# Performance work log

Measured on AMD Instinct MI355X. Metric: run time of the kernel, lower is better.

## Reference

```python
import jax, jax.numpy as jnp
import numpy as np

B, S, H, NH = 2, 2048, 2048, 16
HD = H // NH  # head_dim = 128


def setup_inputs() -> dict:
    key = jax.random.key(0)
    ks = jax.random.split(key, 6)
    scale = 1.0 / np.sqrt(H)
    hidden_state = jax.random.normal(ks[0], (B, S, H), dtype=jnp.float32)
    # upper-triangular (strictly above diagonal) = 1 -> masked positions
    causal_mask = jnp.triu(jnp.ones((S, S), dtype=jnp.float32), k=1)[None, None]
    Wq = jax.random.normal(ks[1], (H, H), dtype=jnp.float32) * scale
    Wk = jax.random.normal(ks[2], (H, H), dtype=jnp.float32) * scale
    Wv = jax.random.normal(ks[3], (H, H), dtype=jnp.float32) * scale
    Wo = jax.random.normal(ks[4], (H, H), dtype=jnp.float32) * scale
    zeros = jnp.zeros((H,), dtype=jnp.float32)
    return {"hidden_state": hidden_state, "causal_mask": causal_mask,
            "Wq": Wq, "bq": zeros, "Wk": Wk, "bk": zeros,
            "Wv": Wv, "bv": zeros, "Wo": Wo, "bo": zeros}


def reference(hidden_state, causal_mask, Wq, bq, Wk, bk, Wv, bv, Wo, bo):
    b, s, h = hidden_state.shape
    q = (hidden_state @ Wq.T + bq).reshape(b, s, NH, HD).transpose(0, 2, 1, 3)  # [B,NH,S,HD]
    k = (hidden_state @ Wk.T + bk).reshape(b, s, NH, HD).transpose(0, 2, 1, 3)
    v = (hidden_state @ Wv.T + bv).reshape(b, s, NH, HD).transpose(0, 2, 1, 3)
    scores = jnp.einsum('bhqd,bhkd->bhqk', q, k) / jnp.sqrt(jnp.float32(HD))
    scores = scores + causal_mask * (-1e9)
    probs = jax.nn.softmax(scores, axis=-1)
    out = jnp.einsum('bhqk,bhkd->bhqd', probs, v)
    out = out.transpose(0, 2, 1, 3).reshape(b, s, h)
    return out @ Wo.T + bo
```

## Files before the change

kernel.cpp:

```cpp
#include <hip/hip_runtime.h>
#include <hip/hip_bf16.h>
#include <stdint.h>

#define B_   2
#define S_   2048
#define H_   2048
#define NH_  16
#define HD_  128
#define MTOT (B_*S_)

typedef __attribute__((ext_vector_type(8))) short bf16x8;
typedef __attribute__((ext_vector_type(4))) float f32x4;

__device__ __forceinline__ void gload_lds16(const void* g, void* l) {
    __builtin_amdgcn_global_load_lds(
        (const __attribute__((address_space(1))) void*)g,
        (__attribute__((address_space(3))) void*)l, 16, 0, 0);
}

__device__ __forceinline__ unsigned short f2bfu(float x) {
    __hip_bfloat16 h = __float2bfloat16(x);
    return *reinterpret_cast<unsigned short*>(&h);
}
__device__ __forceinline__ int packbf(float a, float b) {
    return (int)f2bfu(a) | ((int)f2bfu(b) << 16);
}

__global__ void castk(const float* __restrict__ in, __hip_bfloat16* __restrict__ out, int n4) {
    int i = blockIdx.x * 256 + threadIdx.x;
    if (i < n4) {
        float4 v = *(const float4*)(in + (size_t)i * 4);
        out[(size_t)i*4 + 0] = __float2bfloat16(v.x);
        out[(size_t)i*4 + 1] = __float2bfloat16(v.y);
        out[(size_t)i*4 + 2] = __float2bfloat16(v.z);
        out[(size_t)i*4 + 3] = __float2bfloat16(v.w);
    }
}

__global__ void castw4(const float* __restrict__ w0, const float* __restrict__ w1,
                       const float* __restrict__ w2, const float* __restrict__ w3,
                       __hip_bfloat16* o0, __hip_bfloat16* o1,
                       __hip_bfloat16* o2, __hip_bfloat16* o3, int n4) {
    const float* in; __hip_bfloat16* out;
    switch (blockIdx.y) {
        case 0:  in = w0; out = o0; break;
        case 1:  in = w1; out = o1; break;
        case 2:  in = w2; out = o2; break;
        default: in = w3; out = o3; break;
    }
    int i = blockIdx.x * 256 + threadIdx.x;
    if (i < n4) {
        float4 v = *(const float4*)(in + (size_t)i * 4);
        out[(size_t)i*4 + 0] = __float2bfloat16(v.x);
        out[(size_t)i*4 + 1] = __float2bfloat16(v.y);
        out[(size_t)i*4 + 2] = __float2bfloat16(v.z);
        out[(size_t)i*4 + 3] = __float2bfloat16(v.w);
    }
}

template<int SMEMB, int BF16OUT>
__device__ __forceinline__ void gemm_body(const __hip_bfloat16* __restrict__ Ablk,
                                          const __hip_bfloat16* __restrict__ Wblk,
                                          const float* __restrict__ bias,
                                          void* __restrict__ Cout,
                                          int N, int K, int br, int bc, bool vt)
{
    __shared__ __align__(16) char smem[SMEMB];
    __hip_bfloat16* As = (__hip_bfloat16*)smem;
    __hip_bfloat16* Bs = (__hip_bfloat16*)(smem + 8192);

    const int tid  = threadIdx.x;
    const int wave = tid >> 6, lane = tid & 63;
    const int quad = lane >> 4, l16 = lane & 15;
    const int wr = wave >> 1, wc = wave & 1;

    f32x4 acc[4][4] = {};

    for (int k0 = 0; k0 < K; k0 += 32) {
#pragma unroll
        for (int t = 0; t < 2; ++t) {
            int c = t * 256 + wave * 64 + lane;
            int row = c >> 2, cc = c & 3;
            int base = (t * 256 + wave * 64) * 16;
            gload_lds16(Ablk + (size_t)row * K + k0 + cc * 8, (char*)As + base);
            gload_lds16(Wblk + (size_t)row * K + k0 + cc * 8, (char*)Bs + base);
        }
        __syncthreads();

        bf16x8 af[4], bf[4];
#pragma unroll
        for (int i = 0; i < 4; ++i)
            af[i] = *(const bf16x8*)&As[(wr * 64 + i * 16 + l16) * 32 + quad * 8];
#pragma unroll
        for (int j = 0; j < 4; ++j)
            bf[j] = *(const bf16x8*)&Bs[(wc * 64 + j * 16 + l16) * 32 + quad * 8];

#pragma unroll
        for (int i = 0; i < 4; ++i)
#pragma unroll
            for (int j = 0; j < 4; ++j)
                acc[i][j] = __builtin_amdgcn_mfma_f32_16x16x32_bf16(af[i], bf[j], acc[i][j], 0, 0, 0);
        __syncthreads();
    }

    if (BF16OUT && vt) {
        __hip_bfloat16* Ls = (__hip_bfloat16*)smem;
#pragma unroll
        for (int j = 0; j < 4; ++j) {
            int d = wc * 64 + j * 16 + l16;
            float bv = bias[bc * 128 + d];
#pragma unroll
            for (int i = 0; i < 4; ++i) {
                int t0 = wr * 64 + i * 16 + quad * 4;
#pragma unroll
                for (int r = 0; r < 4; ++r)
                    Ls[d * 136 + t0 + r] = __float2bfloat16(acc[i][j][r] + bv);
            }
        }
        __syncthreads();
        const int bq = br >> 4;
        const int s0 = (br & 15) * 128;
        __hip_bfloat16* VT = (__hip_bfloat16*)Cout;
        const size_t rowbase = (size_t)(bq * 16 + bc) * 128;
#pragma unroll
        for (int rep = 0; rep < 8; ++rep) {
            int L = rep * 256 + tid;
            int d = L >> 4, tch = L & 15;
            bf16x8 v = *(const bf16x8*)&Ls[d * 136 + tch * 8];
            *(bf16x8*)(VT + (rowbase + d) * (size_t)S_ + s0 + tch * 8) = v;
        }
        return;
    }

#pragma unroll
    for (int i = 0; i < 4; ++i) {
        int row = br * 128 + wr * 64 + i * 16 + quad * 4;
#pragma unroll
        for (int j = 0; j < 4; ++j) {
            int col = bc * 128 + wc * 64 + j * 16 + l16;
            float bv = bias[col];
#pragma unroll
            for (int r = 0; r < 4; ++r) {
                float v = acc[i][j][r] + bv;
                if (BF16OUT)
                    ((__hip_bfloat16*)Cout)[(size_t)(row + r) * N + col] = __float2bfloat16(v);
                else
                    ((float*)Cout)[(size_t)(row + r) * N + col] = v;
            }
        }
    }
}

__global__ __launch_bounds__(256)
void gemm_qkv(const __hip_bfloat16* __restrict__ X,
              const __hip_bfloat16* __restrict__ Wq, const __hip_bfloat16* __restrict__ Wk,
              const __hip_bfloat16* __restrict__ Wv,
              const float* __restrict__ bq, const float* __restrict__ bk,
              const float* __restrict__ bv,
              __hip_bfloat16* Qo, __hip_bfloat16* Ko, __hip_bfloat16* VTo)
{
    const int sel = blockIdx.x >> 4;
    const int bc  = blockIdx.x & 15;
    const int br  = blockIdx.y;
    const __hip_bfloat16* W = (sel == 0) ? Wq : (sel == 1) ? Wk : Wv;
    const float* bias       = (sel == 0) ? bq : (sel == 1) ? bk : bv;
    void* out               = (sel == 0) ? (void*)Qo : (sel == 1) ? (void*)Ko : (void*)VTo;
    gemm_body<34816, 1>(X + (size_t)(br * 128) * H_, W + (size_t)(bc * 128) * H_,
                        bias, out, H_, H_, br, bc, sel == 2);
}

__global__ __launch_bounds__(256)
void gemm_out(const __hip_bfloat16* __restrict__ A, const __hip_bfloat16* __restrict__ W,
              const float* __restrict__ bias, float* __restrict__ C)
{
    gemm_body<16384, 0>(A + (size_t)(blockIdx.y * 128) * H_, W + (size_t)(blockIdx.x * 128) * H_,
                        bias, C, H_, H_, blockIdx.y, blockIdx.x, false);
}

__global__ __launch_bounds__(256)
void attn_kernel(const __hip_bfloat16* __restrict__ Q,
                 const __hip_bfloat16* __restrict__ K,
                 const __hip_bfloat16* __restrict__ VT,
                 __hip_bfloat16* __restrict__ O)
{
    __shared__ __align__(16) char Ks[16384];
    __shared__ __align__(16) char Vt[16384];

    const int tid  = threadIdx.x;
    const int wave = tid >> 6, lane = tid & 63;
    const int quad = lane >> 4, l16 = lane & 15;

    const int lid = blockIdx.x;
    const int xcd = lid & 7;
    const int q   = lid >> 3;
    const int bh  = ((q >> 5) << 3) | xcd;
    const int qb  = 31 - (q & 31);
    const int b   = bh >> 4, h = bh & 15;

    const size_t headoff = (size_t)b * S_ * H_ + (size_t)h * HD_;
    const __hip_bfloat16* Qp  = Q + headoff;
    const __hip_bfloat16* Kp  = K + headoff;
    const __hip_bfloat16* Vtp = VT + (size_t)(b * 16 + h) * 128 * S_;

    const float scale = 0.08838834764831843f;
    const int A0 = (((quad & 1) * 2) * 16 + l16) * 4;
    const int A1 = A0 + 64;
    const bool hiq = (quad >= 2);

    const int qrow_local = wave * 16;
    const int qrow = qb * 64 + qrow_local;

    bf16x8 qf[4];
#pragma unroll
    for (int kd = 0; kd < 4; ++kd)
        qf[kd] = *(const bf16x8*)(Qp + (size_t)(qrow + l16) * H_ + kd * 32 + quad * 8);

    f32x4 oacc[8] = {};
    float mi = -1e30f, li = 0.0f;

#pragma unroll
    for (int t = 0; t < 4; ++t) {
        int c = wave * 256 + t * 64 + lane;
        int krow = c >> 4, kpos = c & 15;
        gload_lds16(Kp + (size_t)krow * H_ + (kpos ^ (krow & 7)) * 8,
                    &Ks[(wave * 256 + t * 64) * 16]);
        int vrow = c >> 3, vpos = c & 7;
        gload_lds16(Vtp + (size_t)vrow * S_ + (vpos ^ (vrow & 7)) * 8,
                    &Vt[(wave * 256 + t * 64) * 16]);
    }
    __syncthreads();

    for (int kb = 0; kb <= qb; ++kb) {
        const bool more = (kb < qb);

        f32x4 sacc[4] = {};
#pragma unroll
        for (int cb = 0; cb < 4; ++cb) {
#pragma unroll
            for (int kd = 0; kd < 4; ++kd) {
                int row = cb * 16 + l16;
                int pos = (4 * kd + quad) ^ (l16 & 7);
                bf16x8 kf = *(const bf16x8*)&Ks[row * 256 + pos * 16];
                sacc[cb] = __builtin_amdgcn_mfma_f32_16x16x32_bf16(kf, qf[kd], sacc[cb], 0, 0, 0);
            }
        }

        __syncthreads();

        if (more) {
            const __hip_bfloat16* Kn = Kp + (size_t)(kb + 1) * 64 * H_;
#pragma unroll
            for (int t = 0; t < 4; ++t) {
                int c = wave * 256 + t * 64 + lane;
                int krow = c >> 4, kpos = c & 15;
                gload_lds16(Kn + (size_t)krow * H_ + (kpos ^ (krow & 7)) * 8,
                            &Ks[(wave * 256 + t * 64) * 16]);
            }
        }

        const bool diag = (kb == qb);
        float p[4][4];
        float tm = -1e30f;
#pragma unroll
        for (int cb = 0; cb < 4; ++cb)
#pragma unroll
            for (int r = 0; r < 4; ++r) {
                float s = sacc[cb][r] * scale;
                if (diag) {
                    int keyl = cb * 16 + quad * 4 + r;
                    if (keyl > qrow_local + l16) s = -1e30f;
                }
                p[cb][r] = s;
                tm = fmaxf(tm, s);
            }
        tm = fmaxf(tm, __shfl_xor(tm, 16));
        tm = fmaxf(tm, __shfl_xor(tm, 32));
        float mnew = fmaxf(mi, tm);
        float sum = 0.0f;
#pragma unroll
        for (int cb = 0; cb < 4; ++cb)
#pragma unroll
            for (int r = 0; r < 4; ++r) {
                float e = __expf(p[cb][r] - mnew);
                p[cb][r] = e;
                sum += e;
            }
        sum += __shfl_xor(sum, 16);
        sum += __shfl_xor(sum, 32);
        float alpha = __expf(mi - mnew);
        li = li * alpha + sum;
        mi = mnew;

        float ar[4];
#pragma unroll
        for (int r = 0; r < 4; ++r)
            ar[r] = __shfl(alpha, quad * 4 + r);
#pragma unroll
        for (int db = 0; db < 8; ++db)
#pragma unroll
            for (int r = 0; r < 4; ++r)
                oacc[db][r] *= ar[r];

        int Pp[4][2];
#pragma unroll
        for (int cb = 0; cb < 4; ++cb) {
            Pp[cb][0] = packbf(p[cb][0], p[cb][1]);
            Pp[cb][1] = packbf(p[cb][2], p[cb][3]);
        }
        bf16x8 pf[2];
#pragma unroll
        for (int ks = 0; ks < 2; ++ks) {
            int c0 = 2 * ks, c1 = 2 * ks + 1;
            int d0 = __builtin_amdgcn_ds_bpermute(A0, Pp[c0][0]);
            int e0 = __builtin_amdgcn_ds_bpermute(A0, Pp[c1][0]);
            int d1 = __builtin_amdgcn_ds_bpermute(A0, Pp[c0][1]);
            int e1 = __builtin_amdgcn_ds_bpermute(A0, Pp[c1][1]);
            int d2 = __builtin_amdgcn_ds_bpermute(A1, Pp[c0][0]);
            int e2 = __builtin_amdgcn_ds_bpermute(A1, Pp[c1][0]);
            int d3 = __builtin_amdgcn_ds_bpermute(A1, Pp[c0][1]);
            int e3 = __builtin_amdgcn_ds_bpermute(A1, Pp[c1][1]);
            union { int i[4]; bf16x8 v; } u;
            u.i[0] = hiq ? e0 : d0;
            u.i[1] = hiq ? e1 : d1;
            u.i[2] = hiq ? e2 : d2;
            u.i[3] = hiq ? e3 : d3;
            pf[ks] = u.v;
        }

#pragma unroll
        for (int ks = 0; ks < 2; ++ks) {
#pragma unroll
            for (int db = 0; db < 8; ++db) {
                int vrow = db * 16 + l16;
                int vpos = (ks * 4 + quad) ^ (l16 & 7);
                bf16x8 vf = *(const bf16x8*)&Vt[vrow * 128 + vpos * 16];
                oacc[db] = __builtin_amdgcn_mfma_f32_16x16x32_bf16(pf[ks], vf, oacc[db], 0, 0, 0);
            }
        }

        __syncthreads();

        if (more) {
            const int vcol = (kb + 1) * 64;
#pragma unroll
            for (int t = 0; t < 4; ++t) {
                int c = wave * 256 + t * 64 + lane;
                int vrow = c >> 3, vpos = c & 7;
                gload_lds16(Vtp + (size_t)vrow * S_ + vcol + (vpos ^ (vrow & 7)) * 8,
                            &Vt[(wave * 256 + t * 64) * 16]);
            }
        }
    }

    float lr[4];
#pragma unroll
    for (int r = 0; r < 4; ++r)
        lr[r] = __shfl(li, quad * 4 + r);
#pragma unroll
    for (int db = 0; db < 8; ++db)
#pragma unroll
        for (int r = 0; r < 4; ++r) {
            float v = oacc[db][r] / lr[r];
            size_t row = (size_t)b * S_ + qrow + quad * 4 + r;
            O[row * H_ + h * HD_ + db * 16 + l16] = __float2bfloat16(v);
        }
}

extern "C" void kernel_launch(void* const* d_in, const int* in_sizes, int n_in,
                              void* d_out, int out_size, void* d_ws, size_t ws_size,
                              hipStream_t stream)
{
    const float* hs = (const float*)d_in[0];
    const float* Wq = (const float*)d_in[2];
    const float* bq = (const float*)d_in[3];
    const float* Wk = (const float*)d_in[4];
    const float* bk = (const float*)d_in[5];
    const float* Wv = (const float*)d_in[6];
    const float* bv = (const float*)d_in[7];
    const float* Wo = (const float*)d_in[8];
    const float* bo = (const float*)d_in[9];

    const size_t szX = (size_t)MTOT * H_;
    const size_t szW = (size_t)H_ * H_;

    __hip_bfloat16* Xbf = (__hip_bfloat16*)d_ws;
    __hip_bfloat16* Wqb = Xbf + szX;
    __hip_bfloat16* Wkb = Wqb + szW;
    __hip_bfloat16* Wvb = Wkb + szW;
    __hip_bfloat16* Wob = Wvb + szW;
    __hip_bfloat16* Qb  = Wob + szW;
    __hip_bfloat16* Kb  = Qb + szX;
    __hip_bfloat16* VTb = Kb + szX;

    castk<<<(int)((szX/4 + 255)/256), 256, 0, stream>>>(hs, Xbf, (int)(szX/4));
    dim3 wgrid((unsigned)((szW/4 + 255)/256), 4);
    castw4<<<wgrid, 256, 0, stream>>>(Wq, Wk, Wv, Wo, Wqb, Wkb, Wvb, Wob, (int)(szW/4));

    gemm_qkv<<<dim3(48, 32), 256, 0, stream>>>(Xbf, Wqb, Wkb, Wvb, bq, bk, bv, Qb, Kb, VTb);

    attn_kernel<<<dim3(1024), 256, 0, stream>>>(Qb, Kb, VTb, Xbf);

    gemm_out<<<dim3(16, 32), 256, 0, stream>>>(Xbf, Wob, bo, (float*)d_out);
}
```

Baseline: 411.7 us.

## Replace QKV GEMM with 256x256-tile 8-wave pipelined kernel and add MFMA priority hints

Swaps the 128x128 QKV projection GEMM for a new kernel that computes 256x256 tiles with 512 threads. It uses 128KB of LDS with double-buffered A/B halves, staged global-to-LDS loads interleaved across eight phases, explicit waitcnt/barrier control, an XCD-aware block swizzle, and a vectorized transposed V store. It also wraps the attention kernel's MFMA loops in s_setprio to favour matrix work. The larger tile cuts redundant operand loads. The cost is only 384 blocks and heavy LDS use, which limits occupancy, and the hand-written waitcnt sequence could create race hazards.

```diff
diff --git a/kernel.cpp b/kernel.cpp
--- a/kernel.cpp
+++ b/kernel.cpp
@@ -10,6 +10,7 @@
 #define MTOT (B_*S_)
 
 typedef __attribute__((ext_vector_type(8))) short bf16x8;
+typedef __attribute__((ext_vector_type(4))) short bf16x4;
 typedef __attribute__((ext_vector_type(4))) float f32x4;
 
 __device__ __forceinline__ void gload_lds16(const void* g, void* l) {
@@ -25,6 +26,10 @@
 __device__ __forceinline__ int packbf(float a, float b) {
     return (int)f2bfu(a) | ((int)f2bfu(b) << 16);
 }
+
+#define BAR()  asm volatile("s_barrier" ::: "memory")
+#define WLG0() asm volatile("s_waitcnt lgkmcnt(0)" ::: "memory")
+#define WVM(n) asm volatile("s_waitcnt vmcnt(" #n ")" ::: "memory")
 
 __global__ void castk(const float* __restrict__ in, __hip_bfloat16* __restrict__ out, int n4) {
     int i = blockIdx.x * 256 + threadIdx.x;
@@ -152,29 +157,170 @@
 }
 
 __global__ __launch_bounds__(256)
-void gemm_qkv(const __hip_bfloat16* __restrict__ X,
-              const __hip_bfloat16* __restrict__ Wq, const __hip_bfloat16* __restrict__ Wk,
-              const __hip_bfloat16* __restrict__ Wv,
-              const float* __restrict__ bq, const float* __restrict__ bk,
-              const float* __restrict__ bv,
-              __hip_bfloat16* Qo, __hip_bfloat16* Ko, __hip_bfloat16* VTo)
-{
-    const int sel = blockIdx.x >> 4;
-    const int bc  = blockIdx.x & 15;
-    const int br  = blockIdx.y;
-    const __hip_bfloat16* W = (sel == 0) ? Wq : (sel == 1) ? Wk : Wv;
-    const float* bias       = (sel == 0) ? bq : (sel == 1) ? bk : bv;
-    void* out               = (sel == 0) ? (void*)Qo : (sel == 1) ? (void*)Ko : (void*)VTo;
-    gemm_body<34816, 1>(X + (size_t)(br * 128) * H_, W + (size_t)(bc * 128) * H_,
-                        bias, out, H_, H_, br, bc, sel == 2);
-}
-
-__global__ __launch_bounds__(256)
 void gemm_out(const __hip_bfloat16* __restrict__ A, const __hip_bfloat16* __restrict__ W,
               const float* __restrict__ bias, float* __restrict__ C)
 {
     gemm_body<16384, 0>(A + (size_t)(blockIdx.y * 128) * H_, W + (size_t)(blockIdx.x * 128) * H_,
                         bias, C, H_, H_, blockIdx.y, blockIdx.x, false);
+}
+
+__global__ __launch_bounds__(512, 2)
+void gemm_qkv8(const __hip_bfloat16* __restrict__ X,
+               const __hip_bfloat16* __restrict__ Wq, const __hip_bfloat16* __restrict__ Wk,
+               const __hip_bfloat16* __restrict__ Wv,
+               const float* __restrict__ bq, const float* __restrict__ bk,
+               const float* __restrict__ bv,
+               __hip_bfloat16* __restrict__ Qo, __hip_bfloat16* __restrict__ Ko,
+               __hip_bfloat16* __restrict__ VTo)
+{
+    __shared__ __align__(16) char smem[131072];
+
+    const int bid = blockIdx.x;
+    const int swz = (bid & 7) * 48 + (bid >> 3);
+    const int sel = swz >> 7;
+    const int rem = swz & 127;
+    const int bm  = rem & 15;
+    const int bn  = rem >> 4;
+
+    const __hip_bfloat16* W = (sel == 0) ? Wq : (sel == 1) ? Wk : Wv;
+    const float* bias       = (sel == 0) ? bq : (sel == 1) ? bk : bv;
+
+    const int tid  = threadIdx.x;
+    const int wave = tid >> 6, lane = tid & 63;
+    const int quad = lane >> 4, l16 = lane & 15;
+    const int wr = wave >> 2, wc = wave & 3;
+
+    const int ro = l16 * 64;
+    const int co = (((l16 & 8) ? ((quad * 8) ^ 16) : (quad * 8)) << 1);
+
+    int r0, c0, r1, c1;
+    {
+        int D = tid * 16;
+        int rg = D >> 11, cg = (D >> 10) & 1;
+        int rr = (D >> 6) & 15, c = (D & 63) >> 1;
+        int cs = (rr & 8) ? (c ^ 16) : c;
+        r0 = rg * 16 + rr;  c0 = cg * 32 + cs;
+        D = 8192 + tid * 16;
+        rg = D >> 11; cg = (D >> 10) & 1;
+        rr = (D >> 6) & 15; c = (D & 63) >> 1;
+        cs = (rr & 8) ? (c ^ 16) : c;
+        r1 = rg * 16 + rr;  c1 = cg * 32 + cs;
+    }
+
+    const __hip_bfloat16* Xp = X + (size_t)(bm * 256) * H_;
+    const __hip_bfloat16* Wp = W + (size_t)(bn * 256) * H_;
+
+    char* const A0h = smem + wr * 16384;
+    char* const A1h = smem + 32768 + wr * 16384;
+    char* const B0h = smem + 65536 + (wc >> 1) * 16384;
+    char* const B1h = smem + 98304 + (wc >> 1) * 16384;
+    const int bsub = (wc & 1) * 4;
+
+    auto STG = [&](char* ldsb, const __hip_bfloat16* g) {
+        gload_lds16(g + (size_t)r0 * H_ + c0, ldsb + wave * 1024);
+        gload_lds16(g + (size_t)r1 * H_ + c1, ldsb + 8192 + wave * 1024);
+    };
+    auto SRC = [&](const __hip_bfloat16* P, int t, int hf) {
+        return P + (size_t)(hf * 128) * H_ + (size_t)t * 64;
+    };
+
+    f32x4 acc[8][4] = {};
+
+    STG(smem,                 SRC(Xp, 0, 0));
+    STG(smem + 16384,         SRC(Xp, 0, 1));
+    STG(smem + 65536,         SRC(Wp, 0, 0));
+    STG(smem + 65536 + 16384, SRC(Wp, 0, 1));
+    STG(smem + 98304,         SRC(Wp, 1, 0));
+    STG(smem + 98304 + 16384, SRC(Wp, 1, 1));
+    WVM(4);
+    BAR();
+
+    const int NIT = H_ / 128;
+    bf16x8 bfr[4][2];
+    for (int j = 0; j < NIT; ++j) {
+        const bool more = (j < NIT - 1);
+        const int t1 = 2 * j + 1;
+#pragma unroll
+        for (int ph = 0; ph < 8; ++ph) {
+            const int p = ph & 3;
+            char* aA = (ph < 4) ? A0h : A1h;
+            char* aB = (ph < 4) ? B0h : B1h;
+
+            if (p == 0) {
+#pragma unroll
+                for (int jj = 0; jj < 4; ++jj)
+#pragma unroll
+                    for (int kk = 0; kk < 2; ++kk)
+                        bfr[jj][kk] = *(const bf16x8*)(aB + ((bsub + jj) * 2 + kk) * 1024 + ro + co);
+            }
+            bf16x8 af[2][2];
+#pragma unroll
+            for (int i2 = 0; i2 < 2; ++i2)
+#pragma unroll
+                for (int kk = 0; kk < 2; ++kk)
+                    af[i2][kk] = *(const bf16x8*)(aA + ((2 * p + i2) * 2 + kk) * 1024 + ro + co);
+
+            if (ph == 0) { STG(smem + 32768, SRC(Xp, t1, 0));
+                           STG(smem + 49152, SRC(Xp, t1, 1)); }
+            else if (ph == 1 && more) STG(smem + 65536,          SRC(Wp, t1 + 1, 0));
+            else if (ph == 2 && more) STG(smem + 65536 + 16384,  SRC(Wp, t1 + 1, 1));
+            else if (ph == 4 && more) STG(smem,                  SRC(Xp, t1 + 1, 0));
+            else if (ph == 5 && more) STG(smem + 16384,          SRC(Xp, t1 + 1, 1));
+            else if (ph == 6 && more) STG(smem + 98304,          SRC(Wp, t1 + 2, 0));
+            else if (ph == 7 && more) STG(smem + 98304 + 16384,  SRC(Wp, t1 + 2, 1));
+
+            if (ph == 3) { if (more) { WVM(4); } else { WVM(0); } }
+            if (ph == 7 && more) { WVM(4); }
+
+            BAR();
+            WLG0();
+            __builtin_amdgcn_sched_barrier(0);
+            __builtin_amdgcn_s_setprio(1);
+#pragma unroll
+            for (int kk = 0; kk < 2; ++kk)
+#pragma unroll
+                for (int i2 = 0; i2 < 2; ++i2)
+#pragma unroll
+                    for (int jj = 0; jj < 4; ++jj)
+                        acc[2 * p + i2][jj] = __builtin_amdgcn_mfma_f32_16x16x32_bf16(
+                            af[i2][kk], bfr[jj][kk], acc[2 * p + i2][jj], 0, 0, 0);
+            __builtin_amdgcn_s_setprio(0);
+            BAR();
+        }
+    }
+
+    if (sel < 2) {
+        __hip_bfloat16* out = (sel == 0) ? Qo : Ko;
+#pragma unroll
+        for (int i = 0; i < 8; ++i) {
+            int row = bm * 256 + wr * 128 + i * 16 + quad * 4;
+#pragma unroll
+            for (int jj = 0; jj < 4; ++jj) {
+                int col = bn * 256 + wc * 64 + jj * 16 + l16;
+                float bv = bias[col];
+#pragma unroll
+                for (int r = 0; r < 4; ++r)
+                    out[(size_t)(row + r) * H_ + col] = __float2bfloat16(acc[i][jj][r] + bv);
+            }
+        }
+    } else {
+#pragma unroll
+        for (int i = 0; i < 8; ++i) {
+            int tok = bm * 256 + wr * 128 + i * 16 + quad * 4;
+            int b = tok >> 11, s = tok & (S_ - 1);
+#pragma unroll
+            for (int jj = 0; jj < 4; ++jj) {
+                int col = bn * 256 + wc * 64 + jj * 16 + l16;
+                int h = col >> 7, d = col & 127;
+                float bv = bias[col];
+                bf16x4 v;
+#pragma unroll
+                for (int r = 0; r < 4; ++r)
+                    v[r] = (short)f2bfu(acc[i][jj][r] + bv);
+                *(bf16x4*)(VTo + ((size_t)(b * 16 + h) * 128 + d) * S_ + s) = v;
+            }
+        }
+    }
 }
 
 __global__ __launch_bounds__(256)
@@ -234,6 +380,7 @@
         const bool more = (kb < qb);
 
         f32x4 sacc[4] = {};
+        __builtin_amdgcn_s_setprio(1);
 #pragma unroll
         for (int cb = 0; cb < 4; ++cb) {
 #pragma unroll
@@ -244,6 +391,7 @@
                 sacc[cb] = __builtin_amdgcn_mfma_f32_16x16x32_bf16(kf, qf[kd], sacc[cb], 0, 0, 0);
             }
         }
+        __builtin_amdgcn_s_setprio(0);
 
         __syncthreads();
 
@@ -327,6 +475,7 @@
             pf[ks] = u.v;
         }
 
+        __builtin_amdgcn_s_setprio(1);
 #pragma unroll
         for (int ks = 0; ks < 2; ++ks) {
 #pragma unroll
@@ -337,6 +486,7 @@
                 oacc[db] = __builtin_amdgcn_mfma_f32_16x16x32_bf16(pf[ks], vf, oacc[db], 0, 0, 0);
             }
         }
+        __builtin_amdgcn_s_setprio(0);
 
         __syncthreads();
 
@@ -396,7 +546,7 @@
     dim3 wgrid((unsigned)((szW/4 + 255)/256), 4);
     castw4<<<wgrid, 256, 0, stream>>>(Wq, Wk, Wv, Wo, Wqb, Wkb, Wvb, Wob, (int)(szW/4));
 
-    gemm_qkv<<<dim3(48, 32), 256, 0, stream>>>(Xbf, Wqb, Wkb, Wvb, bq, bk, bv, Qb, Kb, VTb);
+    gemm_qkv8<<<dim3(384), 512, 0, stream>>>(Xbf, Wqb, Wkb, Wvb, bq, bk, bv, Qb, Kb, VTb);
 
     attn_kernel<<<dim3(1024), 256, 0, stream>>>(Qb, Kb, VTb, Xbf);
 
```

Result: slower. 421.8 us (+2.5%).
